# Performance work log

Hardware: AMD Instinct MI355X
Metric: run time of the kernel (lower is better)

Reference implementation:

```python
import jax, jax.numpy as jnp
import numpy as np


def setup_inputs() -> dict:
    key = jax.random.key(0)
    kq, kk, kv = jax.random.split(key, 3)
    B, S, D = 16, 2048, 128
    q = jax.random.normal(kq, (B, S, D), dtype=jnp.float32)
    k = jax.random.normal(kk, (B, S, D), dtype=jnp.float32)
    v = jax.random.normal(kv, (B, S, D), dtype=jnp.float32)
    return {"q": q, "k": k, "v": v}


def reference(q, k, v):
    # scores: [B, Sq, Sk] = q @ k^T, scaled by 1/sqrt(D)
    scale = k.shape[-1] ** -0.5
    scores = jnp.einsum("bqd,bkd->bqk", q, k) * scale
    attention = jax.nn.softmax(scores, axis=2)  # Softmax(dim=2)
    # dropout p=0.0 -> identity (eval-mode equivalent)
    context = jnp.einsum("bqk,bkd->bqd", attention, v)
    return (context, attention)
```

## Files before the change

kernel.cpp:

```cpp
#include <hip/hip_runtime.h>
#include <stdint.h>

#define BB 16
#define SS 2048
#define DD 128

typedef __attribute__((ext_vector_type(8))) short short8;
typedef __attribute__((ext_vector_type(4))) short short4v;
typedef __attribute__((ext_vector_type(4))) float float4v;

__device__ __forceinline__ short f2b(float f){
  unsigned u = __float_as_uint(f);
  u += 0x7fffu + ((u >> 16) & 1u);
  return (short)(u >> 16);
}
__device__ __forceinline__ float b2f(short h){
  return __uint_as_float(((unsigned)(unsigned short)h) << 16);
}

__global__ __launch_bounds__(256) void cvt_k(const float* __restrict__ k, short* __restrict__ kb){
  int i = blockIdx.x * 256 + threadIdx.x;
  float4v f = ((const float4v*)k)[i];
  short4v h;
  h[0]=f2b(f[0]); h[1]=f2b(f[1]); h[2]=f2b(f[2]); h[3]=f2b(f[3]);
  ((short4v*)kb)[i] = h;
}

__global__ __launch_bounds__(256) void trans_v(const float* __restrict__ v, short* __restrict__ vt){
  __shared__ float tile[32][33];
  int blk = blockIdx.x;
  int b   = blk >> 8;
  int rem = blk & 255;
  int k0 = (rem >> 2) << 5;
  int d0 = (rem & 3) << 5;
  int r = threadIdx.x >> 5, c = threadIdx.x & 31;
  const float* vb = v + (size_t)b * SS * DD;
  #pragma unroll
  for (int i=0;i<4;i++)
    tile[r + 8*i][c] = vb[(size_t)(k0 + r + 8*i) * DD + d0 + c];
  __syncthreads();
  short* vtb = vt + (size_t)b * DD * SS;
  #pragma unroll
  for (int i=0;i<4;i++)
    vtb[(size_t)(d0 + r + 8*i) * SS + k0 + c] = f2b(tile[c][r + 8*i]);
}

__global__ __launch_bounds__(512, 4) void attn(const float* __restrict__ q,
                                               const short* __restrict__ kb,
                                               const short* __restrict__ vt,
                                               float* __restrict__ out){
  __shared__ __align__(16) short Pt[16 * 2056];
  __shared__ float red[8][16];
  __shared__ float invl[16];

  const float scale = 0.08838834764831845f;
  int blk = blockIdx.x;
  int swz = ((blk & 7) << 8) + (blk >> 3);
  int b   = swz >> 7;
  int q0  = (swz & 127) << 4;
  int tid = threadIdx.x;
  int w    = tid >> 6;
  int L    = tid & 63;
  int m    = L & 15;
  int quad = L >> 4;
  int lw   = w << 4;

  short8 aq[4];
  {
    const float* qrow = q + (size_t)(b * SS + q0 + m) * DD;
    #pragma unroll
    for (int fi=0; fi<4; fi++){
      int d0 = fi*32 + quad*8;
      short8 h;
      #pragma unroll
      for (int j=0;j<8;j++) h[j] = f2b(qrow[d0 + j]);
      aq[fi] = h;
    }
  }

  const short* kbB = kb + (size_t)b * SS * DD;

  float rs[4] = {0.f, 0.f, 0.f, 0.f};
  for (int kt=0; kt<16; kt++){
    int k0 = kt << 7;
    const short* kg = kbB + (size_t)(k0 + lw + m) * DD + quad*8;
    short8 b0 = *(const short8*)(kg);
    short8 b1 = *(const short8*)(kg + 32);
    short8 b2 = *(const short8*)(kg + 64);
    short8 b3 = *(const short8*)(kg + 96);
    float4v a0 = {0.f,0.f,0.f,0.f}, a1 = {0.f,0.f,0.f,0.f};
    a0 = __builtin_amdgcn_mfma_f32_16x16x32_bf16(aq[0], b0, a0, 0,0,0);
    a1 = __builtin_amdgcn_mfma_f32_16x16x32_bf16(aq[1], b1, a1, 0,0,0);
    a0 = __builtin_amdgcn_mfma_f32_16x16x32_bf16(aq[2], b2, a0, 0,0,0);
    a1 = __builtin_amdgcn_mfma_f32_16x16x32_bf16(aq[3], b3, a1, 0,0,0);

    int col = k0 + lw + m;
    #pragma unroll
    for (int r=0;r<4;r++){
      float p = __expf((a0[r] + a1[r]) * scale);
      short h = f2b(p);
      rs[r] += b2f(h);
      Pt[(quad*4 + r) * 2056 + col] = h;
    }
  }

  #pragma unroll
  for (int r=0;r<4;r++){
    float s = rs[r];
    s += __shfl_xor(s, 1);
    s += __shfl_xor(s, 2);
    s += __shfl_xor(s, 4);
    s += __shfl_xor(s, 8);
    rs[r] = s;
  }
  if (m == 0){
    #pragma unroll
    for (int r=0;r<4;r++) red[w][quad*4 + r] = rs[r];
  }
  __syncthreads();
  if (tid < 16){
    float s = 0.f;
    #pragma unroll
    for (int j=0;j<8;j++) s += red[j][tid];
    invl[tid] = 1.0f / s;
  }
  __syncthreads();

  float* ctx = out;
  float* att = out + (size_t)BB * SS * DD;
  float* attBase = att + (size_t)(b * SS + q0) * SS;
  const short* vtB = vt + (size_t)b * DD * SS;

  float4v o0 = {0.f,0.f,0.f,0.f}, o1 = {0.f,0.f,0.f,0.f};
  int row2 = tid >> 5;
  int c4   = (tid & 31) << 2;
  float il2 = 0.f;
  const short* vg = vtB + (size_t)(lw + m) * SS + quad*8;

  for (int kt=0; kt<16; kt++){
    int k0 = kt << 7;
    {
      short4v h = *(const short4v*)&Pt[row2 * 2056 + k0 + c4];
      il2 = invl[row2];
      float4v f;
      f[0] = b2f(h[0]) * il2; f[1] = b2f(h[1]) * il2;
      f[2] = b2f(h[2]) * il2; f[3] = b2f(h[3]) * il2;
      __builtin_nontemporal_store(f, (float4v*)(attBase + (size_t)row2 * SS + k0 + c4));
    }
    #pragma unroll
    for (int kk=0; kk<4; kk++){
      short8 af = *(const short8*)&Pt[m * 2056 + k0 + kk*32 + quad*8];
      short8 bf = *(const short8*)(vg + k0 + kk*32);
      if (kk & 1) o1 = __builtin_amdgcn_mfma_f32_16x16x32_bf16(af, bf, o1, 0,0,0);
      else        o0 = __builtin_amdgcn_mfma_f32_16x16x32_bf16(af, bf, o0, 0,0,0);
    }
  }

  #pragma unroll
  for (int r=0;r<4;r++){
    int row = quad*4 + r;
    __builtin_nontemporal_store((o0[r] + o1[r]) * invl[row],
                                &ctx[(size_t)(b * SS + q0 + row) * DD + lw + m]);
  }
}

extern "C" void kernel_launch(void* const* d_in, const int* in_sizes, int n_in,
                              void* d_out, int out_size, void* d_ws, size_t ws_size,
                              hipStream_t stream) {
  const float* q = (const float*)d_in[0];
  const float* k = (const float*)d_in[1];
  const float* v = (const float*)d_in[2];
  float* out = (float*)d_out;
  short* kbf = (short*)d_ws;
  short* vtr = kbf + (size_t)BB * SS * DD;
  cvt_k  <<<(BB*SS*DD/4)/256, 256, 0, stream>>>(k, kbf);
  trans_v<<<BB*(SS/32)*(DD/32), 256, 0, stream>>>(v, vtr);
  attn   <<<BB*(SS/16), 512, 0, stream>>>(q, kbf, vtr, out);
}
```

Measured before the change: 515.9 us.

## Prefetch K and V fragments two tiles ahead with register double buffering

Both the QK^T and PV loops now keep two tiles of K/V MFMA operands in registers and issue the loads for tile kt+2 before computing tile kt, hiding global-load latency behind MFMA and exp work. MFMA sections are wrapped with s_setprio to favor matrix issue, the Q load is vectorized into float4 reads, and invl is read once outside the loop. The cost is higher register pressure under launch_bounds(512,4), which could cause spills or lower occupancy, plus redundant wraparound loads on the final iterations.

```diff
diff --git a/kernel.cpp b/kernel.cpp
--- a/kernel.cpp
+++ b/kernel.cpp
@@ -71,30 +71,41 @@
     #pragma unroll
     for (int fi=0; fi<4; fi++){
       int d0 = fi*32 + quad*8;
+      float4v f0 = *(const float4v*)(qrow + d0);
+      float4v f1 = *(const float4v*)(qrow + d0 + 4);
       short8 h;
-      #pragma unroll
-      for (int j=0;j<8;j++) h[j] = f2b(qrow[d0 + j]);
+      h[0]=f2b(f0[0]); h[1]=f2b(f0[1]); h[2]=f2b(f0[2]); h[3]=f2b(f0[3]);
+      h[4]=f2b(f1[0]); h[5]=f2b(f1[1]); h[6]=f2b(f1[2]); h[7]=f2b(f1[3]);
       aq[fi] = h;
     }
   }
 
-  const short* kbB = kb + (size_t)b * SS * DD;
+  const short* kgBase = kb + (size_t)b * SS * DD + (size_t)(lw + m) * DD + quad*8;
+
+  short8 A0[4], A1[4];
+  #pragma unroll
+  for (int i=0;i<4;i++) A0[i] = *(const short8*)(kgBase + (size_t)0*16384 + i*32);
+  #pragma unroll
+  for (int i=0;i<4;i++) A1[i] = *(const short8*)(kgBase + (size_t)1*16384 + i*32);
 
   float rs[4] = {0.f, 0.f, 0.f, 0.f};
   for (int kt=0; kt<16; kt++){
-    int k0 = kt << 7;
-    const short* kg = kbB + (size_t)(k0 + lw + m) * DD + quad*8;
-    short8 b0 = *(const short8*)(kg);
-    short8 b1 = *(const short8*)(kg + 32);
-    short8 b2 = *(const short8*)(kg + 64);
-    short8 b3 = *(const short8*)(kg + 96);
+    short8 cur[4];
+    #pragma unroll
+    for (int i=0;i<4;i++){ cur[i] = A0[i]; A0[i] = A1[i]; }
+    int ktn = kt + 2; if (ktn > 15) ktn = kt & 1;
+    #pragma unroll
+    for (int i=0;i<4;i++) A1[i] = *(const short8*)(kgBase + (size_t)ktn*16384 + i*32);
+
     float4v a0 = {0.f,0.f,0.f,0.f}, a1 = {0.f,0.f,0.f,0.f};
-    a0 = __builtin_amdgcn_mfma_f32_16x16x32_bf16(aq[0], b0, a0, 0,0,0);
-    a1 = __builtin_amdgcn_mfma_f32_16x16x32_bf16(aq[1], b1, a1, 0,0,0);
-    a0 = __builtin_amdgcn_mfma_f32_16x16x32_bf16(aq[2], b2, a0, 0,0,0);
-    a1 = __builtin_amdgcn_mfma_f32_16x16x32_bf16(aq[3], b3, a1, 0,0,0);
-
-    int col = k0 + lw + m;
+    __builtin_amdgcn_s_setprio(1);
+    a0 = __builtin_amdgcn_mfma_f32_16x16x32_bf16(aq[0], cur[0], a0, 0,0,0);
+    a1 = __builtin_amdgcn_mfma_f32_16x16x32_bf16(aq[1], cur[1], a1, 0,0,0);
+    a0 = __builtin_amdgcn_mfma_f32_16x16x32_bf16(aq[2], cur[2], a0, 0,0,0);
+    a1 = __builtin_amdgcn_mfma_f32_16x16x32_bf16(aq[3], cur[3], a1, 0,0,0);
+    __builtin_amdgcn_s_setprio(0);
+
+    int col = (kt << 7) + lw + m;
     #pragma unroll
     for (int r=0;r<4;r++){
       float p = __expf((a0[r] + a1[r]) * scale);
@@ -129,31 +140,44 @@
   float* ctx = out;
   float* att = out + (size_t)BB * SS * DD;
   float* attBase = att + (size_t)(b * SS + q0) * SS;
-  const short* vtB = vt + (size_t)b * DD * SS;
-
-  float4v o0 = {0.f,0.f,0.f,0.f}, o1 = {0.f,0.f,0.f,0.f};
+
+  const short* vgBase = vt + (size_t)b * DD * SS + (size_t)(lw + m) * SS + quad*8;
   int row2 = tid >> 5;
   int c4   = (tid & 31) << 2;
-  float il2 = 0.f;
-  const short* vg = vtB + (size_t)(lw + m) * SS + quad*8;
-
+  float il2 = invl[row2];
+
+  short8 B0[4], B1[4];
+  #pragma unroll
+  for (int i=0;i<4;i++) B0[i] = *(const short8*)(vgBase + (size_t)0*128 + i*32);
+  #pragma unroll
+  for (int i=0;i<4;i++) B1[i] = *(const short8*)(vgBase + (size_t)1*128 + i*32);
+
+  float4v o0 = {0.f,0.f,0.f,0.f}, o1 = {0.f,0.f,0.f,0.f};
   for (int kt=0; kt<16; kt++){
     int k0 = kt << 7;
+    short8 cur[4];
+    #pragma unroll
+    for (int i=0;i<4;i++){ cur[i] = B0[i]; B0[i] = B1[i]; }
+    int ktn = kt + 2; if (ktn > 15) ktn = kt & 1;
+    #pragma unroll
+    for (int i=0;i<4;i++) B1[i] = *(const short8*)(vgBase + (size_t)ktn*128 + i*32);
+
     {
       short4v h = *(const short4v*)&Pt[row2 * 2056 + k0 + c4];
-      il2 = invl[row2];
       float4v f;
       f[0] = b2f(h[0]) * il2; f[1] = b2f(h[1]) * il2;
       f[2] = b2f(h[2]) * il2; f[3] = b2f(h[3]) * il2;
       __builtin_nontemporal_store(f, (float4v*)(attBase + (size_t)row2 * SS + k0 + c4));
     }
+
+    __builtin_amdgcn_s_setprio(1);
     #pragma unroll
     for (int kk=0; kk<4; kk++){
       short8 af = *(const short8*)&Pt[m * 2056 + k0 + kk*32 + quad*8];
-      short8 bf = *(const short8*)(vg + k0 + kk*32);
-      if (kk & 1) o1 = __builtin_amdgcn_mfma_f32_16x16x32_bf16(af, bf, o1, 0,0,0);
-      else        o0 = __builtin_amdgcn_mfma_f32_16x16x32_bf16(af, bf, o0, 0,0,0);
-    }
+      if (kk & 1) o1 = __builtin_amdgcn_mfma_f32_16x16x32_bf16(af, cur[kk], o1, 0,0,0);
+      else        o0 = __builtin_amdgcn_mfma_f32_16x16x32_bf16(af, cur[kk], o0, 0,0,0);
+    }
+    __builtin_amdgcn_s_setprio(0);
   }
 
   #pragma unroll
```

Result: slower. 528.3 us (+2.4%).

## Double-buffer K and V tiles in LDS via async global-to-LDS loads

Applied to the files above, without the earlier changes.

K and V^T tiles are now staged into a double-buffered, XOR-swizzled LDS buffer with global_load_lds, waited on with vmcnt and barriers, instead of each wave loading its MFMA operands directly from global memory. The attention-matrix stores move out of the PV loop to after it, and Q loads are vectorized. The aim is to overlap memory fetches with MFMA work and to share K/V tiles across waves. In exchange the kernel uses 64KB more LDS and the launch bound drops to 2 blocks per CU, lowering occupancy, and it adds two barriers per iteration.

```diff
diff --git a/kernel.cpp b/kernel.cpp
--- a/kernel.cpp
+++ b/kernel.cpp
@@ -16,6 +16,12 @@
 }
 __device__ __forceinline__ float b2f(short h){
   return __uint_as_float(((unsigned)(unsigned short)h) << 16);
+}
+
+__device__ __forceinline__ void gload16(const short* g, short* l){
+  __builtin_amdgcn_global_load_lds(
+      (const __attribute__((address_space(1))) void*)g,
+      (__attribute__((address_space(3))) void*)l, 16, 0, 0);
 }
 
 __global__ __launch_bounds__(256) void cvt_k(const float* __restrict__ k, short* __restrict__ kb){
@@ -45,10 +51,11 @@
     vtb[(size_t)(d0 + r + 8*i) * SS + k0 + c] = f2b(tile[c][r + 8*i]);
 }
 
-__global__ __launch_bounds__(512, 4) void attn(const float* __restrict__ q,
+__global__ __launch_bounds__(512, 2) void attn(const float* __restrict__ q,
                                                const short* __restrict__ kb,
                                                const short* __restrict__ vt,
                                                float* __restrict__ out){
+  __shared__ __align__(16) short KVs[2 * 128 * 128];
   __shared__ __align__(16) short Pt[16 * 2056];
   __shared__ float red[8][16];
   __shared__ float invl[16];
@@ -71,30 +78,67 @@
     #pragma unroll
     for (int fi=0; fi<4; fi++){
       int d0 = fi*32 + quad*8;
+      float4v f0 = *(const float4v*)(qrow + d0);
+      float4v f1 = *(const float4v*)(qrow + d0 + 4);
       short8 h;
-      #pragma unroll
-      for (int j=0;j<8;j++) h[j] = f2b(qrow[d0 + j]);
+      h[0]=f2b(f0[0]); h[1]=f2b(f0[1]); h[2]=f2b(f0[2]); h[3]=f2b(f0[3]);
+      h[4]=f2b(f1[0]); h[5]=f2b(f1[1]); h[6]=f2b(f1[2]); h[7]=f2b(f1[3]);
       aq[fi] = h;
     }
   }
 
   const short* kbB = kb + (size_t)b * SS * DD;
+  const short* vtB = vt + (size_t)b * DD * SS;
+
+  auto stageK = [&](int t, int buf){
+    const short* gsrc = kbB + ((size_t)t << 14);
+    #pragma unroll
+    for (int j=0;j<4;j++){
+      int c   = (w << 2) + j;
+      int row = (c << 2) + (L >> 4);
+      int col16 = (L & 15) ^ (row & 7);
+      gload16(gsrc + (size_t)row * DD + (col16 << 3),
+              &KVs[buf * 16384 + (c << 9)]);
+    }
+  };
+  auto stageV = [&](int t, int buf){
+    int k0 = t << 7;
+    #pragma unroll
+    for (int j=0;j<4;j++){
+      int c   = (w << 2) + j;
+      int row = (c << 2) + (L >> 4);
+      int col16 = (L & 15) ^ (row & 7);
+      gload16(vtB + (size_t)row * SS + k0 + (col16 << 3),
+              &KVs[buf * 16384 + (c << 9)]);
+    }
+  };
 
   float rs[4] = {0.f, 0.f, 0.f, 0.f};
-  for (int kt=0; kt<16; kt++){
-    int k0 = kt << 7;
-    const short* kg = kbB + (size_t)(k0 + lw + m) * DD + quad*8;
-    short8 b0 = *(const short8*)(kg);
-    short8 b1 = *(const short8*)(kg + 32);
-    short8 b2 = *(const short8*)(kg + 64);
-    short8 b3 = *(const short8*)(kg + 96);
+  stageK(0, 0);
+  stageK(1, 1);
+  int sw = m & 7;
+  for (int t=0; t<16; t++){
+    int buf = t & 1;
+    if (t < 15) asm volatile("s_waitcnt vmcnt(4)" ::: "memory");
+    else        asm volatile("s_waitcnt vmcnt(0)" ::: "memory");
+    __builtin_amdgcn_s_barrier();
+    asm volatile("" ::: "memory");
+
+    const short* base = &KVs[buf * 16384 + (lw + m) * 128];
+    short8 b0 = *(const short8*)(base + (((quad     ) ^ sw) << 3));
+    short8 b1 = *(const short8*)(base + (((quad +  4) ^ sw) << 3));
+    short8 b2 = *(const short8*)(base + (((quad +  8) ^ sw) << 3));
+    short8 b3 = *(const short8*)(base + (((quad + 12) ^ sw) << 3));
+
     float4v a0 = {0.f,0.f,0.f,0.f}, a1 = {0.f,0.f,0.f,0.f};
+    __builtin_amdgcn_s_setprio(1);
     a0 = __builtin_amdgcn_mfma_f32_16x16x32_bf16(aq[0], b0, a0, 0,0,0);
     a1 = __builtin_amdgcn_mfma_f32_16x16x32_bf16(aq[1], b1, a1, 0,0,0);
     a0 = __builtin_amdgcn_mfma_f32_16x16x32_bf16(aq[2], b2, a0, 0,0,0);
     a1 = __builtin_amdgcn_mfma_f32_16x16x32_bf16(aq[3], b3, a1, 0,0,0);
-
-    int col = k0 + lw + m;
+    __builtin_amdgcn_s_setprio(0);
+
+    int col = (t << 7) + lw + m;
     #pragma unroll
     for (int r=0;r<4;r++){
       float p = __expf((a0[r] + a1[r]) * scale);
@@ -102,6 +146,10 @@
       rs[r] += b2f(h);
       Pt[(quad*4 + r) * 2056 + col] = h;
     }
+
+    asm volatile("s_waitcnt lgkmcnt(0)" ::: "memory");
+    __builtin_amdgcn_s_barrier();
+    if (t + 2 < 16) stageK(t + 2, buf);
   }
 
   #pragma unroll
@@ -126,41 +174,61 @@
   }
   __syncthreads();
 
+  stageV(0, 0);
+  stageV(1, 1);
+  float4v o0 = {0.f,0.f,0.f,0.f}, o1 = {0.f,0.f,0.f,0.f};
+  for (int t=0; t<16; t++){
+    int buf = t & 1;
+    if (t < 15) asm volatile("s_waitcnt vmcnt(4)" ::: "memory");
+    else        asm volatile("s_waitcnt vmcnt(0)" ::: "memory");
+    __builtin_amdgcn_s_barrier();
+    asm volatile("" ::: "memory");
+
+    const short* vb = &KVs[buf * 16384 + (lw + m) * 128];
+    int k0 = t << 7;
+    short8 af0 = *(const short8*)&Pt[m * 2056 + k0 +  0 + quad*8];
+    short8 af1 = *(const short8*)&Pt[m * 2056 + k0 + 32 + quad*8];
+    short8 af2 = *(const short8*)&Pt[m * 2056 + k0 + 64 + quad*8];
+    short8 af3 = *(const short8*)&Pt[m * 2056 + k0 + 96 + quad*8];
+    short8 bf0 = *(const short8*)(vb + (((quad     ) ^ sw) << 3));
+    short8 bf1 = *(const short8*)(vb + (((quad +  4) ^ sw) << 3));
+    short8 bf2 = *(const short8*)(vb + (((quad +  8) ^ sw) << 3));
+    short8 bf3 = *(const short8*)(vb + (((quad + 12) ^ sw) << 3));
+
+    __builtin_amdgcn_s_setprio(1);
+    o0 = __builtin_amdgcn_mfma_f32_16x16x32_bf16(af0, bf0, o0, 0,0,0);
+    o1 = __builtin_amdgcn_mfma_f32_16x16x32_bf16(af1, bf1, o1, 0,0,0);
+    o0 = __builtin_amdgcn_mfma_f32_16x16x32_bf16(af2, bf2, o0, 0,0,0);
+    o1 = __builtin_amdgcn_mfma_f32_16x16x32_bf16(af3, bf3, o1, 0,0,0);
+    __builtin_amdgcn_s_setprio(0);
+
+    asm volatile("s_waitcnt lgkmcnt(0)" ::: "memory");
+    __builtin_amdgcn_s_barrier();
+    if (t + 2 < 16) stageV(t + 2, buf);
+  }
+
   float* ctx = out;
   float* att = out + (size_t)BB * SS * DD;
-  float* attBase = att + (size_t)(b * SS + q0) * SS;
-  const short* vtB = vt + (size_t)b * DD * SS;
-
-  float4v o0 = {0.f,0.f,0.f,0.f}, o1 = {0.f,0.f,0.f,0.f};
-  int row2 = tid >> 5;
-  int c4   = (tid & 31) << 2;
-  float il2 = 0.f;
-  const short* vg = vtB + (size_t)(lw + m) * SS + quad*8;
-
-  for (int kt=0; kt<16; kt++){
-    int k0 = kt << 7;
-    {
+  #pragma unroll
+  for (int r=0;r<4;r++){
+    int row = quad*4 + r;
+    __builtin_nontemporal_store((o0[r] + o1[r]) * invl[row],
+                                &ctx[(size_t)(b * SS + q0 + row) * DD + lw + m]);
+  }
+  {
+    float* attBase = att + (size_t)(b * SS + q0) * SS;
+    int row2 = tid >> 5;
+    int c4   = (tid & 31) << 2;
+    float il2 = invl[row2];
+    #pragma unroll
+    for (int kt=0; kt<16; kt++){
+      int k0 = kt << 7;
       short4v h = *(const short4v*)&Pt[row2 * 2056 + k0 + c4];
-      il2 = invl[row2];
       float4v f;
       f[0] = b2f(h[0]) * il2; f[1] = b2f(h[1]) * il2;
       f[2] = b2f(h[2]) * il2; f[3] = b2f(h[3]) * il2;
       __builtin_nontemporal_store(f, (float4v*)(attBase + (size_t)row2 * SS + k0 + c4));
     }
-    #pragma unroll
-    for (int kk=0; kk<4; kk++){
-      short8 af = *(const short8*)&Pt[m * 2056 + k0 + kk*32 + quad*8];
-      short8 bf = *(const short8*)(vg + k0 + kk*32);
-      if (kk & 1) o1 = __builtin_amdgcn_mfma_f32_16x16x32_bf16(af, bf, o1, 0,0,0);
-      else        o0 = __builtin_amdgcn_mfma_f32_16x16x32_bf16(af, bf, o0, 0,0,0);
-    }
-  }
-
-  #pragma unroll
-  for (int r=0;r<4;r++){
-    int row = quad*4 + r;
-    __builtin_nontemporal_store((o0[r] + o1[r]) * invl[row],
-                                &ctx[(size_t)(b * SS + q0 + row) * DD + lw + m]);
   }
 }
 
```

New measurement: 462.1 us. 10.4% less time.
